# Optimization experiments

Hardware: AMD Instinct MI355X
Metric: run time of the kernel (lower is better)

The kernel has to match this reference:

```python
import jax, jax.numpy as jnp
import numpy as np
from jax import lax

GROUPS = 32
EPS = 1e-5
NEG_SLOPE = 0.1


def group_norm(x, gamma, beta):
    # x: (B, C, H, W); GroupNorm over (C//G, H, W) per group
    B, C, H, W = x.shape
    xr = x.reshape(B, GROUPS, C // GROUPS, H, W)
    mean = xr.mean(axis=(2, 3, 4), keepdims=True)
    var = xr.var(axis=(2, 3, 4), keepdims=True)
    xn = ((xr - mean) * lax.rsqrt(var + EPS)).reshape(B, C, H, W)
    return xn * gamma[None, :, None, None] + beta[None, :, None, None]


def conv3x3(x, w, b):
    y = lax.conv_general_dilated(x, w, (1, 1), 'SAME',
                                 dimension_numbers=('NCHW', 'OIHW', 'NCHW'))
    return y + b[None, :, None, None]


def leaky_relu(x):
    return jnp.where(x >= 0, x, NEG_SLOPE * x)


def setup_inputs() -> dict:
    key = jax.random.key(0)
    ks = jax.random.split(key, 12)
    B, C, H, W = 16, 128, 128, 128
    emb = 128
    s = 0.05
    return {
        'x': jax.random.normal(ks[0], (B, C, H, W), jnp.float32),
        'time_emb': jax.random.normal(ks[1], (B, emb), jnp.float32),
        'k_v': jax.random.normal(ks[2], (B, 64), jnp.float32),
        'gn1_g': jnp.ones((C,), jnp.float32),
        'gn1_b': jnp.zeros((C,), jnp.float32),
        'conv1_w': jax.random.normal(ks[3], (C, C, 3, 3), jnp.float32) * s,
        'conv1_b': jax.random.normal(ks[4], (C,), jnp.float32) * s,
        'nf_w': jax.random.normal(ks[5], (C, emb), jnp.float32) * s,
        'nf_b': jax.random.normal(ks[6], (C,), jnp.float32) * s,
        'kW1': jax.random.normal(ks[7], (64, 64), jnp.float32) * s,
        'kW2': jax.random.normal(ks[8], (C * 9, 64), jnp.float32) * s,
        'daconv_w': jax.random.normal(ks[9], (C, C, 3, 3), jnp.float32) * s,
        'daconv_b': jax.random.normal(ks[10], (C,), jnp.float32) * s,
    }


def reference(x, time_emb, k_v, gn1_g, gn1_b, conv1_w, conv1_b,
              nf_w, nf_b, kW1, kW2, daconv_w, daconv_b):
    B, C, H, W = x.shape
    # block1: GroupNorm -> Swish -> Conv3x3
    h = group_norm(x, gn1_g, gn1_b)
    h = h * jax.nn.sigmoid(h)
    h = conv3x3(h, conv1_w, conv1_b)
    # FeatureWiseAffine (use_affine_level=False): h + Linear(time_emb)
    h = h + (time_emb @ nf_w.T + nf_b)[:, :, None, None]
    # DABlock: its GroupNorm+Swish output is discarded in the original code,
    # so only DA_conv(h, k_v) matters.
    # dynamic per-sample depthwise kernel: (B, 64) -> (B*C, 1, 3, 3)
    kern = (leaky_relu(k_v @ kW1.T) @ kW2.T).reshape(B * C, 1, 3, 3)
    xr = h.reshape(1, B * C, H, W)
    dyn = lax.conv_general_dilated(xr, kern, (1, 1), 'SAME',
                                   dimension_numbers=('NCHW', 'OIHW', 'NCHW'),
                                   feature_group_count=B * C)
    dyn = leaky_relu(dyn).reshape(B, C, H, W)
    h = dyn + conv3x3(h, daconv_w, daconv_b)
    # residual: dim == dim_out -> res_conv = Identity
    return h + x
```

## Files before the change

### kernel.cpp

```cpp
#include <hip/hip_runtime.h>
#include <hip/hip_bf16.h>
#include <math.h>
#include <stdint.h>

typedef unsigned short u16;
typedef __attribute__((ext_vector_type(8))) short bfrag;
typedef __attribute__((ext_vector_type(4))) float f32x4;
typedef __attribute__((ext_vector_type(8))) unsigned short u16x8;
typedef __attribute__((ext_vector_type(4))) unsigned short u16x4;

#define BB 16
#define CC 128
#define HH 128
#define WW 128
#define EPSV 1e-5f
#define NEG 0.1f
#define PW 130

__device__ __forceinline__ float bf2f(u16 u) {
    unsigned int x = ((unsigned int)u) << 16;
    return __builtin_bit_cast(float, x);
}
__device__ __forceinline__ u16 f2bf(float f) {
    unsigned int x = __builtin_bit_cast(unsigned int, f);
    unsigned int r = x + 0x7fffu + ((x >> 16) & 1u);
    return (u16)(r >> 16);
}
__device__ __forceinline__ void gload_lds16(const void* g, void* l) {
    __builtin_amdgcn_global_load_lds(
        (const __attribute__((address_space(1))) void*)g,
        (__attribute__((address_space(3))) void*)l, 16, 0, 0);
}

__global__ __launch_bounds__(256)
void prep_kernel(const float* __restrict__ x, float* __restrict__ stats,
                 const float* __restrict__ w1, const float* __restrict__ w2,
                 u16* __restrict__ w1t, u16* __restrict__ w2t,
                 u16* __restrict__ hact, u16* __restrict__ hbuf,
                 const float* __restrict__ te, const float* __restrict__ nfw,
                 const float* __restrict__ nfbias, const float* __restrict__ c1b,
                 float* __restrict__ biastot,
                 const float* __restrict__ kv, const float* __restrict__ kw1,
                 const float* __restrict__ kw2, float* __restrict__ kern_t) {
    __shared__ float rs[8];
    __shared__ float s_t1[64];
    const int blk = blockIdx.x;
    const int tid = threadIdx.x;

    if (blk < 512) {
        const int bg = blk;
        const float* base = x + (size_t)bg * 65536;
        float s1 = 0.f, s2 = 0.f;
        for (int i = tid; i < 16384; i += 256) {
            float4 v = *(const float4*)&base[i * 4];
            s1 += v.x + v.y + v.z + v.w;
            s2 += v.x * v.x + v.y * v.y + v.z * v.z + v.w * v.w;
        }
        #pragma unroll
        for (int off = 32; off > 0; off >>= 1) {
            s1 += __shfl_down(s1, off);
            s2 += __shfl_down(s2, off);
        }
        const int wid = tid >> 6, lane = tid & 63;
        if (lane == 0) { rs[wid * 2] = s1; rs[wid * 2 + 1] = s2; }
        __syncthreads();
        if (tid == 0) {
            s1 = rs[0] + rs[2] + rs[4] + rs[6];
            s2 = rs[1] + rs[3] + rs[5] + rs[7];
            float mean = s1 * (1.f / 65536.f);
            float var  = s2 * (1.f / 65536.f) - mean * mean;
            stats[2 * bg]     = mean;
            stats[2 * bg + 1] = rsqrtf(var + EPSV);
        }
    } else if (blk < 1088) {
        int idx = (blk - 512) * 256 + tid;
        int e  = idx & 7;
        int co = (idx >> 3) & 127;
        int g  = (idx >> 10) & 3;
        int ck = (idx >> 12) & 3;
        int t  = idx >> 14;
        int src = (co * 128 + (ck * 32 + g * 8 + e)) * 9 + t;
        w1t[idx] = f2bf(w1[src]);
        w2t[idx] = f2bf(w2[src]);
    } else if (blk < 1604) {
        int idx = (blk - 1088) * 256 + tid;
        int cg = idx & 15;
        int t = idx >> 4;
        int b = t / 516, e = t - b * 516;
        int y, xx;
        if (e < 130)      { y = 0;           xx = e; }
        else if (e < 260) { y = 129;         xx = e - 130; }
        else if (e < 388) { y = e - 260 + 1; xx = 0; }
        else              { y = e - 388 + 1; xx = 129; }
        size_t o = (((size_t)b * PW + y) * PW + xx) * 128 + cg * 8;
        u16x8 z = (u16x8)(u16)0;
        *(u16x8*)&hact[o] = z;
        *(u16x8*)&hbuf[o] = z;
    } else if (blk < 1612) {
        int idx = (blk - 1604) * 256 + tid;
        const int b = idx >> 7, c = idx & 127;
        float s = nfbias[c] + c1b[c];
        for (int e = 0; e < 128; ++e) s += te[b * 128 + e] * nfw[c * 128 + e];
        biastot[idx] = s;
    } else {
        const int b = blk - 1612;
        if (tid < 64) {
            float s = 0.f;
            for (int e = 0; e < 64; ++e) s += kv[b * 64 + e] * kw1[tid * 64 + e];
            s_t1[tid] = s >= 0.f ? s : NEG * s;
        }
        __syncthreads();
        for (int i = tid; i < 1152; i += 256) {
            float s = 0.f;
            for (int e = 0; e < 64; ++e) s += s_t1[e] * kw2[(size_t)i * 64 + e];
            int c = i / 9, t = i - c * 9;
            kern_t[((size_t)b * 9 + t) * 128 + c] = s;
        }
    }
}

__global__ __launch_bounds__(256)
void gn_apply_kernel(const float* __restrict__ x, const float* __restrict__ gamma,
                     const float* __restrict__ beta, const float* __restrict__ stats,
                     u16* __restrict__ hact) {
    __shared__ u16 s_t[128 * 128];
    const int tid = threadIdx.x;
    const int y = blockIdx.x & 127, b = blockIdx.x >> 7;
    #pragma unroll
    for (int i = 0; i < 16; ++i) {
        int unit = (i << 8) + tid;
        int c = unit >> 5, xq = unit & 31, xx = xq * 4;
        float4 v = *(const float4*)&x[(((size_t)b * 128 + c) * 128 + y) * 128 + xx];
        int gi = b * 32 + (c >> 2);
        float mean = stats[2 * gi], rstd = stats[2 * gi + 1];
        float ga = gamma[c] * rstd, be = beta[c] - mean * ga;
        float a0 = v.x * ga + be, a1 = v.y * ga + be, a2 = v.z * ga + be, a3 = v.w * ga + be;
        a0 = a0 / (1.f + __expf(-a0)); a1 = a1 / (1.f + __expf(-a1));
        a2 = a2 / (1.f + __expf(-a2)); a3 = a3 / (1.f + __expf(-a3));
        int cs = c ^ ((xq & 15) << 3);
        s_t[(xx + 0) * 128 + cs] = f2bf(a0);
        s_t[(xx + 1) * 128 + cs] = f2bf(a1);
        s_t[(xx + 2) * 128 + cs] = f2bf(a2);
        s_t[(xx + 3) * 128 + cs] = f2bf(a3);
    }
    __syncthreads();
    #pragma unroll
    for (int i = 0; i < 8; ++i) {
        int unit = (i << 8) + tid;
        int xx = unit >> 4, c0 = (unit & 15) * 8;
        int c0s = c0 ^ (((xx >> 2) & 15) << 3);
        u16x8 v = *(const u16x8*)&s_t[xx * 128 + c0s];
        *(u16x8*)&hact[(((size_t)b * PW + y + 1) * PW + (xx + 1)) * 128 + c0] = v;
    }
}

__global__ __launch_bounds__(512, 4)
void conv1_mfma_kernel(const u16* __restrict__ act, const u16* __restrict__ wt,
                       const float* __restrict__ bias, u16* __restrict__ outh) {
    __shared__ __align__(16) u16 s_in[2][1024 * 8];

    const int tid = threadIdx.x;
    const int lane = tid & 63, wid = tid >> 6;
    const int wm = wid & 3, wq = wid >> 2;
    const int l15 = lane & 15, l4 = lane >> 4;

    const int bid0 = blockIdx.x;
    const int bid = ((bid0 & 7) << 8) | (bid0 >> 3);
    const int tx = bid & 7, ty = (bid >> 3) & 15, b = bid >> 7;
    const int x0 = tx * 16, y0 = ty * 8;

    f32x4 acc[2][4];
    #pragma unroll
    for (int mi = 0; mi < 2; ++mi)
        #pragma unroll
        for (int nj = 0; nj < 4; ++nj) acc[mi][nj] = (f32x4)(0.f);

    int in_vofs[2];
    #pragma unroll
    for (int r = 0; r < 2; ++r) {
        int slot = r * 512 + tid;
        if (slot > 719) slot = 719;
        int cik = slot / 180;
        int pos = slot - cik * 180;
        int row = pos / 18, col = pos - row * 18;
        in_vofs[r] = (row * PW + col) * 128 + cik * 8;
    }
    const u16* in_base = act + (((size_t)b * PW + y0) * PW + x0) * 128;

    auto stage_in = [&](int buf, int ci0) {
        #pragma unroll
        for (int r = 0; r < 2; ++r)
            gload_lds16(in_base + ci0 + in_vofs[r],
                        &s_in[buf][(size_t)(r * 512 + (wid << 6)) * 8]);
    };

    const u16* wlane = wt + l4 * 1024 + (wm * 32 + l15) * 8;
    const int bbase = (l4 * 180 + (wq * 4) * 18 + l15) * 8;

    stage_in(0, 0);
    asm volatile("s_waitcnt vmcnt(0)" ::: "memory");
    __builtin_amdgcn_s_barrier();
    __builtin_amdgcn_sched_barrier(0);

    #pragma unroll
    for (int c = 0; c < 4; ++c) {
        if (c > 0) {
            __builtin_amdgcn_s_barrier();
            __builtin_amdgcn_sched_barrier(0);
        }
        if (c < 3) stage_in((c + 1) & 1, (c + 1) * 32);
        __builtin_amdgcn_sched_barrier(0);

        const u16* sb = &s_in[c & 1][0];
        #pragma unroll
        for (int dyr = 0; dyr < 3; ++dyr) {
            #pragma unroll
            for (int dx = 0; dx < 3; ++dx) {
                const u16* wp = wlane + (size_t)(((dyr * 3 + dx) * 4 + c) * 4096);
                bfrag a0 = *(const bfrag*)(wp);
                bfrag a1 = *(const bfrag*)(wp + 128);
                const int bo = bbase + (dyr * 18 + dx) * 8;
                bfrag b0 = *(const bfrag*)&sb[bo];
                bfrag b1 = *(const bfrag*)&sb[bo + 144];
                bfrag b2 = *(const bfrag*)&sb[bo + 288];
                bfrag b3 = *(const bfrag*)&sb[bo + 432];

                __builtin_amdgcn_s_setprio(1);
                acc[0][0] = __builtin_amdgcn_mfma_f32_16x16x32_bf16(a0, b0, acc[0][0], 0, 0, 0);
                acc[0][1] = __builtin_amdgcn_mfma_f32_16x16x32_bf16(a0, b1, acc[0][1], 0, 0, 0);
                acc[0][2] = __builtin_amdgcn_mfma_f32_16x16x32_bf16(a0, b2, acc[0][2], 0, 0, 0);
                acc[0][3] = __builtin_amdgcn_mfma_f32_16x16x32_bf16(a0, b3, acc[0][3], 0, 0, 0);
                acc[1][0] = __builtin_amdgcn_mfma_f32_16x16x32_bf16(a1, b0, acc[1][0], 0, 0, 0);
                acc[1][1] = __builtin_amdgcn_mfma_f32_16x16x32_bf16(a1, b1, acc[1][1], 0, 0, 0);
                acc[1][2] = __builtin_amdgcn_mfma_f32_16x16x32_bf16(a1, b2, acc[1][2], 0, 0, 0);
                acc[1][3] = __builtin_amdgcn_mfma_f32_16x16x32_bf16(a1, b3, acc[1][3], 0, 0, 0);
                __builtin_amdgcn_s_setprio(0);
            }
        }
    }

    const float* bb = bias + b * 128;
    #pragma unroll
    for (int mi = 0; mi < 2; ++mi) {
        const int cb = wm * 32 + mi * 16 + l4 * 4;
        float4 bv4 = *(const float4*)&bb[cb];
        #pragma unroll
        for (int nj = 0; nj < 4; ++nj) {
            int y = y0 + wq * 4 + nj, xx = x0 + l15;
            u16x4 pk;
            pk[0] = f2bf(acc[mi][nj][0] + bv4.x);
            pk[1] = f2bf(acc[mi][nj][1] + bv4.y);
            pk[2] = f2bf(acc[mi][nj][2] + bv4.z);
            pk[3] = f2bf(acc[mi][nj][3] + bv4.w);
            *(u16x4*)&outh[(((size_t)b * PW + y + 1) * PW + (xx + 1)) * 128 + cb] = pk;
        }
    }
}

__global__ __launch_bounds__(512, 2)
void conv2_mfma_kernel(const u16* __restrict__ act, const u16* __restrict__ wt,
                       const float* __restrict__ bias, const float* __restrict__ kern_t,
                       const float* __restrict__ xres, float* __restrict__ outf) {
    __shared__ __align__(16) u16 s_in[2][1536 * 8];
    __shared__ float s_k[1152];

    const int tid = threadIdx.x;
    const int lane = tid & 63, wid = tid >> 6;
    const int wm = wid & 1, wq = wid >> 1;
    const int l15 = lane & 15, l4 = lane >> 4;

    const int bid0 = blockIdx.x;
    const int bid = ((bid0 & 7) << 7) | (bid0 >> 3);
    const int tx = bid & 7;
    const int x0 = tx * 16;
    const int b_  = bid >> 6;
    const int ty_ = (bid >> 3) & 7;
    const int y0_ = ty_ * 16;

    f32x4 acc[4][4];
    #pragma unroll
    for (int mi = 0; mi < 4; ++mi)
        #pragma unroll
        for (int nj = 0; nj < 4; ++nj) acc[mi][nj] = (f32x4)(0.f);

    float dw[2][2][4][4];
    #pragma unroll
    for (int a0 = 0; a0 < 2; ++a0)
        #pragma unroll
        for (int a1 = 0; a1 < 2; ++a1)
            #pragma unroll
            for (int a2 = 0; a2 < 4; ++a2)
                #pragma unroll
                for (int a3 = 0; a3 < 4; ++a3) dw[a0][a1][a2][a3] = 0.f;

    for (int i = tid; i < 1152; i += 512) s_k[i] = kern_t[(size_t)b_ * 1152 + i];
    __syncthreads();

    int in_vofs[3];
    #pragma unroll
    for (int r = 0; r < 3; ++r) {
        int slot = r * 512 + tid;
        int cik = slot / 384;
        int pos = slot - cik * 384;
        if (pos > 323) pos = 323;
        int row = pos / 18, col = pos - row * 18;
        in_vofs[r] = (row * PW + col) * 128 + cik * 8;
    }
    const u16* in_base = act + (((size_t)b_ * PW + y0_) * PW + x0) * 128;
    const int ldst = (wid << 6) * 8;

    auto stage_in = [&](int buf, int ci0) {
        #pragma unroll
        for (int r = 0; r < 3; ++r)
            gload_lds16(in_base + ci0 + in_vofs[r], &s_in[buf][r * 512 * 8 + ldst]);
    };

    const u16* wlane = wt + l4 * 1024 + (wm * 64 + l15) * 8;
    const int bbase = (l4 * 384 + (wq * 4) * 18 + l15) * 8;

    auto dwcomp = [&](int ck, int dyr) {
        if ((ck >> 1) == wm) {
            const int mih = ck & 1;
            const u16* sb = &s_in[ck & 1][0];
            #pragma unroll
            for (int mm = 0; mm < 2; ++mm) {
                const int cik = 2 * mm + (l4 >> 1);
                const int e0 = (l4 & 1) * 4;
                const int cb = ck * 32 + mm * 16 + l4 * 4;
                #pragma unroll
                for (int dx = 0; dx < 3; ++dx) {
                    const int tap = dyr * 3 + dx;
                    float4 kk = *(const float4*)&s_k[tap * 128 + cb];
                    #pragma unroll
                    for (int nj = 0; nj < 4; ++nj) {
                        const int row = wq * 4 + nj + dyr;
                        const int col = l15 + dx;
                        u16x4 hv = *(const u16x4*)
                            &sb[(cik * 384 + row * 18 + col) * 8 + e0];
                        dw[mih][mm][nj][0] += bf2f(hv[0]) * kk.x;
                        dw[mih][mm][nj][1] += bf2f(hv[1]) * kk.y;
                        dw[mih][mm][nj][2] += bf2f(hv[2]) * kk.z;
                        dw[mih][mm][nj][3] += bf2f(hv[3]) * kk.w;
                    }
                }
            }
        }
    };

    stage_in(0, 0);
    asm volatile("s_waitcnt vmcnt(0)" ::: "memory");
    __builtin_amdgcn_s_barrier();
    __builtin_amdgcn_sched_barrier(0);

    #pragma unroll
    for (int c = 0; c < 4; ++c) {
        if (c > 0) {
            __builtin_amdgcn_s_barrier();
        }
        if (c < 3) {
            stage_in((c + 1) & 1, (c + 1) * 32);
            asm volatile("s_waitcnt vmcnt(3)" ::: "memory");
        }
        __builtin_amdgcn_sched_barrier(0);

        const u16* sb = &s_in[c & 1][0];
        #pragma unroll
        for (int dyr = 0; dyr < 3; ++dyr) {
            bfrag wR[3][4];
            #pragma unroll
            for (int dx = 0; dx < 3; ++dx) {
                const u16* wp = wlane + ((dyr * 3 + dx) * 4 + c) * 4096;
                #pragma unroll
                for (int mi = 0; mi < 4; ++mi)
                    wR[dx][mi] = *(const bfrag*)(wp + mi * 128);
            }
            __builtin_amdgcn_s_setprio(1);
            #pragma unroll
            for (int dx = 0; dx < 3; ++dx) {
                const int bo = bbase + (dyr * 18 + dx) * 8;
                bfrag b0 = *(const bfrag*)&sb[bo];
                bfrag b1 = *(const bfrag*)&sb[bo + 144];
                bfrag b2 = *(const bfrag*)&sb[bo + 288];
                bfrag b3 = *(const bfrag*)&sb[bo + 432];

                acc[0][0] = __builtin_amdgcn_mfma_f32_16x16x32_bf16(wR[dx][0], b0, acc[0][0], 0, 0, 0);
                acc[0][1] = __builtin_amdgcn_mfma_f32_16x16x32_bf16(wR[dx][0], b1, acc[0][1], 0, 0, 0);
                acc[0][2] = __builtin_amdgcn_mfma_f32_16x16x32_bf16(wR[dx][0], b2, acc[0][2], 0, 0, 0);
                acc[0][3] = __builtin_amdgcn_mfma_f32_16x16x32_bf16(wR[dx][0], b3, acc[0][3], 0, 0, 0);
                acc[1][0] = __builtin_amdgcn_mfma_f32_16x16x32_bf16(wR[dx][1], b0, acc[1][0], 0, 0, 0);
                acc[1][1] = __builtin_amdgcn_mfma_f32_16x16x32_bf16(wR[dx][1], b1, acc[1][1], 0, 0, 0);
                acc[1][2] = __builtin_amdgcn_mfma_f32_16x16x32_bf16(wR[dx][1], b2, acc[1][2], 0, 0, 0);
                acc[1][3] = __builtin_amdgcn_mfma_f32_16x16x32_bf16(wR[dx][1], b3, acc[1][3], 0, 0, 0);
                acc[2][0] = __builtin_amdgcn_mfma_f32_16x16x32_bf16(wR[dx][2], b0, acc[2][0], 0, 0, 0);
                acc[2][1] = __builtin_amdgcn_mfma_f32_16x16x32_bf16(wR[dx][2], b1, acc[2][1], 0, 0, 0);
                acc[2][2] = __builtin_amdgcn_mfma_f32_16x16x32_bf16(wR[dx][2], b2, acc[2][2], 0, 0, 0);
                acc[2][3] = __builtin_amdgcn_mfma_f32_16x16x32_bf16(wR[dx][2], b3, acc[2][3], 0, 0, 0);
                acc[3][0] = __builtin_amdgcn_mfma_f32_16x16x32_bf16(wR[dx][3], b0, acc[3][0], 0, 0, 0);
                acc[3][1] = __builtin_amdgcn_mfma_f32_16x16x32_bf16(wR[dx][3], b1, acc[3][1], 0, 0, 0);
                acc[3][2] = __builtin_amdgcn_mfma_f32_16x16x32_bf16(wR[dx][3], b2, acc[3][2], 0, 0, 0);
                acc[3][3] = __builtin_amdgcn_mfma_f32_16x16x32_bf16(wR[dx][3], b3, acc[3][3], 0, 0, 0);
            }
            __builtin_amdgcn_s_setprio(0);
            dwcomp(c, dyr);
        }
    }

    #pragma unroll
    for (int mi = 0; mi < 4; ++mi) {
        const int cb = wm * 64 + mi * 16 + l4 * 4;
        float4 bv4 = *(const float4*)&bias[cb];
        #pragma unroll
        for (int nj = 0; nj < 4; ++nj) {
            int y = y0_ + wq * 4 + nj, xx = x0 + l15;
            size_t obase = (((size_t)b_ * 128 + cb) * 128 + y) * 128 + xx;
            #pragma unroll
            for (int j = 0; j < 4; ++j) {
                float d = dw[mi >> 1][mi & 1][nj][j];
                d = d >= 0.f ? d : NEG * d;
                float bj = (j == 0) ? bv4.x : (j == 1) ? bv4.y : (j == 2) ? bv4.z : bv4.w;
                outf[obase + (size_t)j * 16384] =
                    acc[mi][nj][j] + bj + d + xres[obase + (size_t)j * 16384];
            }
        }
    }
}

extern "C" void kernel_launch(void* const* d_in, const int* in_sizes, int n_in,
                              void* d_out, int out_size, void* d_ws, size_t ws_size,
                              hipStream_t stream) {
    const float* x        = (const float*)d_in[0];
    const float* te       = (const float*)d_in[1];
    const float* kv       = (const float*)d_in[2];
    const float* gn1_g    = (const float*)d_in[3];
    const float* gn1_b    = (const float*)d_in[4];
    const float* conv1_w  = (const float*)d_in[5];
    const float* conv1_b  = (const float*)d_in[6];
    const float* nf_w     = (const float*)d_in[7];
    const float* nf_b     = (const float*)d_in[8];
    const float* kW1      = (const float*)d_in[9];
    const float* kW2      = (const float*)d_in[10];
    const float* daconv_w = (const float*)d_in[11];
    const float* daconv_b = (const float*)d_in[12];

    float* out = (float*)d_out;

    float* kern  = (float*)d_ws;
    u16*   w2t   = (u16*)(kern + 18432);
    u16*   hbuf  = (u16*)(kern + 92160);

    u16*   hact    = (u16*)out;
    float* up      = out + 17500160;
    float* stats   = up;
    float* biastot = up + 1024;
    u16*   w1t     = (u16*)(up + 4096);

    prep_kernel<<<dim3(1628), dim3(256), 0, stream>>>(
        x, stats, conv1_w, daconv_w, w1t, w2t, hact, hbuf,
        te, nf_w, nf_b, conv1_b, biastot, kv, kW1, kW2, kern);
    gn_apply_kernel<<<dim3(2048), dim3(256), 0, stream>>>(x, gn1_g, gn1_b, stats, hact);
    conv1_mfma_kernel<<<dim3(2048), dim3(512), 0, stream>>>(hact, w1t, biastot, hbuf);
    conv2_mfma_kernel<<<dim3(1024), dim3(512), 0, stream>>>(
        hbuf, w2t, daconv_b, kern, x, out);
}
```

Before: 290.0 us.

## Shrink conv2 tile to 8x16 pixels with 4x2 warp layout for higher occupancy

Each conv2 block now covers an 8-row by 16-column spatial tile instead of 16x16. The work is split across 4 channel-warps by 2 row-warps, so each warp holds 2x4 accumulators instead of 4x4 and loads its weights per dx instead of preloading all three. The grid doubles to 2048 blocks and launch bounds ask for 4 blocks per CU, aiming to raise occupancy and cut register pressure. The cost is more halo reloading per output and less weight reuse per MFMA.

```diff
diff --git a/kernel.cpp b/kernel.cpp
--- a/kernel.cpp
+++ b/kernel.cpp
@@ -257,76 +257,70 @@
     }
 }
 
-__global__ __launch_bounds__(512, 2)
+__global__ __launch_bounds__(512, 4)
 void conv2_mfma_kernel(const u16* __restrict__ act, const u16* __restrict__ wt,
                        const float* __restrict__ bias, const float* __restrict__ kern_t,
                        const float* __restrict__ xres, float* __restrict__ outf) {
-    __shared__ __align__(16) u16 s_in[2][1536 * 8];
+    __shared__ __align__(16) u16 s_in[2][1024 * 8];
     __shared__ float s_k[1152];
 
     const int tid = threadIdx.x;
     const int lane = tid & 63, wid = tid >> 6;
-    const int wm = wid & 1, wq = wid >> 1;
+    const int wm = wid & 3, wq = wid >> 2;
     const int l15 = lane & 15, l4 = lane >> 4;
 
     const int bid0 = blockIdx.x;
-    const int bid = ((bid0 & 7) << 7) | (bid0 >> 3);
-    const int tx = bid & 7;
-    const int x0 = tx * 16;
-    const int b_  = bid >> 6;
-    const int ty_ = (bid >> 3) & 7;
-    const int y0_ = ty_ * 16;
-
-    f32x4 acc[4][4];
-    #pragma unroll
-    for (int mi = 0; mi < 4; ++mi)
+    const int bid = ((bid0 & 7) << 8) | (bid0 >> 3);
+    const int tx = bid & 7, ty = (bid >> 3) & 15, b = bid >> 7;
+    const int x0 = tx * 16, y0 = ty * 8;
+
+    f32x4 acc[2][4];
+    #pragma unroll
+    for (int mi = 0; mi < 2; ++mi)
         #pragma unroll
         for (int nj = 0; nj < 4; ++nj) acc[mi][nj] = (f32x4)(0.f);
 
-    float dw[2][2][4][4];
-    #pragma unroll
-    for (int a0 = 0; a0 < 2; ++a0)
-        #pragma unroll
-        for (int a1 = 0; a1 < 2; ++a1)
+    float dw[2][4][4];
+    #pragma unroll
+    for (int a1 = 0; a1 < 2; ++a1)
+        #pragma unroll
+        for (int a2 = 0; a2 < 4; ++a2)
             #pragma unroll
-            for (int a2 = 0; a2 < 4; ++a2)
-                #pragma unroll
-                for (int a3 = 0; a3 < 4; ++a3) dw[a0][a1][a2][a3] = 0.f;
-
-    for (int i = tid; i < 1152; i += 512) s_k[i] = kern_t[(size_t)b_ * 1152 + i];
+            for (int a3 = 0; a3 < 4; ++a3) dw[a1][a2][a3] = 0.f;
+
+    for (int i = tid; i < 1152; i += 512) s_k[i] = kern_t[(size_t)b * 1152 + i];
     __syncthreads();
 
-    int in_vofs[3];
-    #pragma unroll
-    for (int r = 0; r < 3; ++r) {
+    int in_vofs[2];
+    #pragma unroll
+    for (int r = 0; r < 2; ++r) {
         int slot = r * 512 + tid;
-        int cik = slot / 384;
-        int pos = slot - cik * 384;
-        if (pos > 323) pos = 323;
+        if (slot > 719) slot = 719;
+        int cik = slot / 180;
+        int pos = slot - cik * 180;
         int row = pos / 18, col = pos - row * 18;
         in_vofs[r] = (row * PW + col) * 128 + cik * 8;
     }
-    const u16* in_base = act + (((size_t)b_ * PW + y0_) * PW + x0) * 128;
-    const int ldst = (wid << 6) * 8;
+    const u16* in_base = act + (((size_t)b * PW + y0) * PW + x0) * 128;
 
     auto stage_in = [&](int buf, int ci0) {
         #pragma unroll
-        for (int r = 0; r < 3; ++r)
-            gload_lds16(in_base + ci0 + in_vofs[r], &s_in[buf][r * 512 * 8 + ldst]);
+        for (int r = 0; r < 2; ++r)
+            gload_lds16(in_base + ci0 + in_vofs[r],
+                        &s_in[buf][(size_t)(r * 512 + (wid << 6)) * 8]);
     };
 
-    const u16* wlane = wt + l4 * 1024 + (wm * 64 + l15) * 8;
-    const int bbase = (l4 * 384 + (wq * 4) * 18 + l15) * 8;
+    const u16* wlane = wt + l4 * 1024 + (wm * 32 + l15) * 8;
+    const int bbase = (l4 * 180 + (wq * 4) * 18 + l15) * 8;
 
     auto dwcomp = [&](int ck, int dyr) {
-        if ((ck >> 1) == wm) {
-            const int mih = ck & 1;
+        if (wm == ck) {
             const u16* sb = &s_in[ck & 1][0];
             #pragma unroll
-            for (int mm = 0; mm < 2; ++mm) {
-                const int cik = 2 * mm + (l4 >> 1);
+            for (int mi = 0; mi < 2; ++mi) {
+                const int cik = mi * 2 + (l4 >> 1);
                 const int e0 = (l4 & 1) * 4;
-                const int cb = ck * 32 + mm * 16 + l4 * 4;
+                const int cb = ck * 32 + mi * 16 + l4 * 4;
                 #pragma unroll
                 for (int dx = 0; dx < 3; ++dx) {
                     const int tap = dyr * 3 + dx;
@@ -336,11 +330,11 @@
                         const int row = wq * 4 + nj + dyr;
                         const int col = l15 + dx;
                         u16x4 hv = *(const u16x4*)
-                            &sb[(cik * 384 + row * 18 + col) * 8 + e0];
-                        dw[mih][mm][nj][0] += bf2f(hv[0]) * kk.x;
-                        dw[mih][mm][nj][1] += bf2f(hv[1]) * kk.y;
-                        dw[mih][mm][nj][2] += bf2f(hv[2]) * kk.z;
-                        dw[mih][mm][nj][3] += bf2f(hv[3]) * kk.w;
+                            &sb[(cik * 180 + row * 18 + col) * 8 + e0];
+                        dw[mi][nj][0] += bf2f(hv[0]) * kk.x;
+                        dw[mi][nj][1] += bf2f(hv[1]) * kk.y;
+                        dw[mi][nj][2] += bf2f(hv[2]) * kk.z;
+                        dw[mi][nj][3] += bf2f(hv[3]) * kk.w;
                     }
                 }
             }
@@ -356,66 +350,56 @@
     for (int c = 0; c < 4; ++c) {
         if (c > 0) {
             __builtin_amdgcn_s_barrier();
+            __builtin_amdgcn_sched_barrier(0);
         }
         if (c < 3) {
             stage_in((c + 1) & 1, (c + 1) * 32);
-            asm volatile("s_waitcnt vmcnt(3)" ::: "memory");
+            asm volatile("s_waitcnt vmcnt(2)" ::: "memory");
+        } else {
+            asm volatile("s_waitcnt vmcnt(0)" ::: "memory");
         }
         __builtin_amdgcn_sched_barrier(0);
 
         const u16* sb = &s_in[c & 1][0];
         #pragma unroll
         for (int dyr = 0; dyr < 3; ++dyr) {
-            bfrag wR[3][4];
             #pragma unroll
             for (int dx = 0; dx < 3; ++dx) {
-                const u16* wp = wlane + ((dyr * 3 + dx) * 4 + c) * 4096;
-                #pragma unroll
-                for (int mi = 0; mi < 4; ++mi)
-                    wR[dx][mi] = *(const bfrag*)(wp + mi * 128);
-            }
-            __builtin_amdgcn_s_setprio(1);
-            #pragma unroll
-            for (int dx = 0; dx < 3; ++dx) {
+                const u16* wp = wlane + (size_t)(((dyr * 3 + dx) * 4 + c) * 4096);
+                bfrag a0 = *(const bfrag*)(wp);
+                bfrag a1 = *(const bfrag*)(wp + 128);
                 const int bo = bbase + (dyr * 18 + dx) * 8;
                 bfrag b0 = *(const bfrag*)&sb[bo];
                 bfrag b1 = *(const bfrag*)&sb[bo + 144];
                 bfrag b2 = *(const bfrag*)&sb[bo + 288];
                 bfrag b3 = *(const bfrag*)&sb[bo + 432];
 
-                acc[0][0] = __builtin_amdgcn_mfma_f32_16x16x32_bf16(wR[dx][0], b0, acc[0][0], 0, 0, 0);
-                acc[0][1] = __builtin_amdgcn_mfma_f32_16x16x32_bf16(wR[dx][0], b1, acc[0][1], 0, 0, 0);
-                acc[0][2] = __builtin_amdgcn_mfma_f32_16x16x32_bf16(wR[dx][0], b2, acc[0][2], 0, 0, 0);
-                acc[0][3] = __builtin_amdgcn_mfma_f32_16x16x32_bf16(wR[dx][0], b3, acc[0][3], 0, 0, 0);
-                acc[1][0] = __builtin_amdgcn_mfma_f32_16x16x32_bf16(wR[dx][1], b0, acc[1][0], 0, 0, 0);
-                acc[1][1] = __builtin_amdgcn_mfma_f32_16x16x32_bf16(wR[dx][1], b1, acc[1][1], 0, 0, 0);
-                acc[1][2] = __builtin_amdgcn_mfma_f32_16x16x32_bf16(wR[dx][1], b2, acc[1][2], 0, 0, 0);
-                acc[1][3] = __builtin_amdgcn_mfma_f32_16x16x32_bf16(wR[dx][1], b3, acc[1][3], 0, 0, 0);
-                acc[2][0] = __builtin_amdgcn_mfma_f32_16x16x32_bf16(wR[dx][2], b0, acc[2][0], 0, 0, 0);
-                acc[2][1] = __builtin_amdgcn_mfma_f32_16x16x32_bf16(wR[dx][2], b1, acc[2][1], 0, 0, 0);
-                acc[2][2] = __builtin_amdgcn_mfma_f32_16x16x32_bf16(wR[dx][2], b2, acc[2][2], 0, 0, 0);
-                acc[2][3] = __builtin_amdgcn_mfma_f32_16x16x32_bf16(wR[dx][2], b3, acc[2][3], 0, 0, 0);
-                acc[3][0] = __builtin_amdgcn_mfma_f32_16x16x32_bf16(wR[dx][3], b0, acc[3][0], 0, 0, 0);
-                acc[3][1] = __builtin_amdgcn_mfma_f32_16x16x32_bf16(wR[dx][3], b1, acc[3][1], 0, 0, 0);
-                acc[3][2] = __builtin_amdgcn_mfma_f32_16x16x32_bf16(wR[dx][3], b2, acc[3][2], 0, 0, 0);
-                acc[3][3] = __builtin_amdgcn_mfma_f32_16x16x32_bf16(wR[dx][3], b3, acc[3][3], 0, 0, 0);
+                __builtin_amdgcn_s_setprio(1);
+                acc[0][0] = __builtin_amdgcn_mfma_f32_16x16x32_bf16(a0, b0, acc[0][0], 0, 0, 0);
+                acc[0][1] = __builtin_amdgcn_mfma_f32_16x16x32_bf16(a0, b1, acc[0][1], 0, 0, 0);
+                acc[0][2] = __builtin_amdgcn_mfma_f32_16x16x32_bf16(a0, b2, acc[0][2], 0, 0, 0);
+                acc[0][3] = __builtin_amdgcn_mfma_f32_16x16x32_bf16(a0, b3, acc[0][3], 0, 0, 0);
+                acc[1][0] = __builtin_amdgcn_mfma_f32_16x16x32_bf16(a1, b0, acc[1][0], 0, 0, 0);
+                acc[1][1] = __builtin_amdgcn_mfma_f32_16x16x32_bf16(a1, b1, acc[1][1], 0, 0, 0);
+                acc[1][2] = __builtin_amdgcn_mfma_f32_16x16x32_bf16(a1, b2, acc[1][2], 0, 0, 0);
+                acc[1][3] = __builtin_amdgcn_mfma_f32_16x16x32_bf16(a1, b3, acc[1][3], 0, 0, 0);
+                __builtin_amdgcn_s_setprio(0);
             }
-            __builtin_amdgcn_s_setprio(0);
             dwcomp(c, dyr);
         }
     }
 
     #pragma unroll
-    for (int mi = 0; mi < 4; ++mi) {
-        const int cb = wm * 64 + mi * 16 + l4 * 4;
+    for (int mi = 0; mi < 2; ++mi) {
+        const int cb = wm * 32 + mi * 16 + l4 * 4;
         float4 bv4 = *(const float4*)&bias[cb];
         #pragma unroll
         for (int nj = 0; nj < 4; ++nj) {
-            int y = y0_ + wq * 4 + nj, xx = x0 + l15;
-            size_t obase = (((size_t)b_ * 128 + cb) * 128 + y) * 128 + xx;
+            int y = y0 + wq * 4 + nj, xx = x0 + l15;
+            size_t obase = (((size_t)b * 128 + cb) * 128 + y) * 128 + xx;
             #pragma unroll
             for (int j = 0; j < 4; ++j) {
-                float d = dw[mi >> 1][mi & 1][nj][j];
+                float d = dw[mi][nj][j];
                 d = d >= 0.f ? d : NEG * d;
                 float bj = (j == 0) ? bv4.x : (j == 1) ? bv4.y : (j == 2) ? bv4.z : bv4.w;
                 outf[obase + (size_t)j * 16384] =
@@ -459,6 +443,6 @@
         te, nf_w, nf_b, conv1_b, biastot, kv, kW1, kW2, kern);
     gn_apply_kernel<<<dim3(2048), dim3(256), 0, stream>>>(x, gn1_g, gn1_b, stats, hact);
     conv1_mfma_kernel<<<dim3(2048), dim3(512), 0, stream>>>(hact, w1t, biastot, hbuf);
-    conv2_mfma_kernel<<<dim3(1024), dim3(512), 0, stream>>>(
+    conv2_mfma_kernel<<<dim3(2048), dim3(512), 0, stream>>>(
         hbuf, w2t, daconv_b, kern, x, out);
 }
```

Result: slower. 374.6 us (+29.2%).
